# Kernel tuning notes

Measured on AMD Instinct MI355X. Metric: run time of the kernel, lower is better.

Reference implementation:

```python
import jax, jax.numpy as jnp
import numpy as np

HEADS = 4

def _pair_msg(H, w2, B, xsrc):
    # H:[E,mid] radial-MLP hidden; w2:[mid,co,ci,nf]; B:[E,m_out,m_in,nf] CG/SH basis; xsrc:[E,ci,m_in]
    tmp = jnp.einsum('epqf,eiq->eipf', B, xsrc)          # basis-weighted input  [E,ci,m_out,nf]
    R = jnp.einsum('eh,hoif->eoif', H, w2)               # per-edge radial weights [E,co,ci,nf]
    return jnp.einsum('eoif,eipf->eop', R, tmp)          # edge message [E,co,m_out]

def _conv_edges(ef, w1, w2_nf1, w2_11, b00, b01, b10, b11, x0s, x1s):
    # pair index p = 2*d_in + d_out; pairs (0,0),(0,1),(1,0) have nf=1, pair (1,1) has nf=3
    H = jax.nn.relu(jnp.einsum('ef,pfh->peh', ef, w1))
    m0 = _pair_msg(H[0], w2_nf1[0][..., None], b00, x0s) + _pair_msg(H[2], w2_nf1[2][..., None], b10, x1s)
    m1 = _pair_msg(H[1], w2_nf1[1][..., None], b01, x0s) + _pair_msg(H[3], w2_11, b11, x1s)
    return m0, m1

def _seg_softmax(z, dst, n):
    m = jax.ops.segment_max(z, dst, num_segments=n)
    m = jnp.where(jnp.isfinite(m), m, 0.0)
    e = jnp.exp(z - m[dst])
    s = jax.ops.segment_sum(e, dst, num_segments=n)
    return e / (s[dst] + 1e-9)

def _norm_se3(x, g, b, eps=1e-3):
    n = jnp.sqrt((x * x).sum(-1) + 1e-12)                # per-channel irrep norm [N,C]
    mu = n.mean(-1, keepdims=True)
    var = ((n - mu) ** 2).mean(-1, keepdims=True)
    ln = (n - mu) / jnp.sqrt(var + 1e-5) * g + b
    return x * (jax.nn.relu(ln) / (n + eps))[..., None]

def _forward(x0, x1, edge_feat, b00, b01, b10, b11, kv_w1, kv_w2_nf1, kv_w2_11,
             wq, wproj, norm_gamma, norm_beta, fc_w1, fc_w2_nf1, fc_w2_11, fc_wself,
             edge_src, edge_dst):
    N = x0.shape[0]
    E = edge_src.shape[0]
    L = kv_w1.shape[0]
    ckv = wq.shape[-1]
    scale = 1.0 / np.sqrt((ckv // HEADS) * 4)            # key feats per head over degrees 0,1 (1+3 comps)
    hs = lambda t: t.reshape(t.shape[0], HEADS, ckv // HEADS, t.shape[-1])
    for l in range(L):
        # AttentionBlockSE3: ConvSE3 -> per-edge key/value; LinearSE3 -> query; seg-softmax attention
        kv0, kv1 = _conv_edges(edge_feat, kv_w1[l], kv_w2_nf1[l], kv_w2_11[l],
                               b00, b01, b10, b11, x0[edge_src], x1[edge_src])
        k0, v0 = kv0[:, :ckv], kv0[:, ckv:]
        k1, v1 = kv1[:, :ckv], kv1[:, ckv:]
        q0 = jnp.einsum('ncm,cd->ndm', x0, wq[l, 0])
        q1 = jnp.einsum('ncm,cd->ndm', x1, wq[l, 1])
        z = (hs(q0)[edge_dst] * hs(k0)).sum((2, 3)) + (hs(q1)[edge_dst] * hs(k1)).sum((2, 3))
        alpha = _seg_softmax(z * scale, edge_dst, N)     # [E,heads]
        a0 = (alpha[:, :, None, None] * hs(v0)).reshape(E, ckv, 1)
        a1 = (alpha[:, :, None, None] * hs(v1)).reshape(E, ckv, 3)
        o0 = jax.ops.segment_sum(a0, edge_dst, num_segments=N)
        o1 = jax.ops.segment_sum(a1, edge_dst, num_segments=N)
        # project concat(attn_out, skip) per degree, then NormSE3
        x0 = jnp.einsum('ncm,cd->ndm', jnp.concatenate([o0, x0], 1), wproj[l, 0])
        x1 = jnp.einsum('ncm,cd->ndm', jnp.concatenate([o1, x1], 1), wproj[l, 1])
        x0 = _norm_se3(x0, norm_gamma[l, 0], norm_beta[l, 0])
        x1 = _norm_se3(x1, norm_gamma[l, 1], norm_beta[l, 1])
    # final ConvSE3 with self-interaction, scatter-aggregated over dst nodes
    m0, m1 = _conv_edges(edge_feat, fc_w1, fc_w2_nf1, fc_w2_11,
                         b00, b01, b10, b11, x0[edge_src], x1[edge_src])
    y0 = jax.ops.segment_sum(m0, edge_dst, num_segments=N) + jnp.einsum('ncm,cd->ndm', x0, fc_wself[0])
    y1 = jax.ops.segment_sum(m1, edge_dst, num_segments=N) + jnp.einsum('ncm,cd->ndm', x1, fc_wself[1])
    return jnp.concatenate([y0.reshape(N, -1), y1.reshape(N, -1)], axis=1)

def setup_inputs() -> dict:
    key = jax.random.key(0)
    ks = jax.random.split(key, 20)
    N, E, C, L = 8192, 131072, 16, 2
    Fe, mid, KV, ckv, Co = 16, 16, 16, 8, 8
    f = lambda k, s, sc=1.0: jax.random.normal(k, s, dtype=jnp.float32) * sc
    return {
        'x0': f(ks[0], (N, C, 1)),
        'x1': f(ks[1], (N, C, 3)),
        'edge_feat': f(ks[2], (E, Fe)),
        'b00': f(ks[3], (E, 1, 1, 1)),
        'b01': f(ks[4], (E, 3, 1, 1)),
        'b10': f(ks[5], (E, 1, 3, 1)),
        'b11': f(ks[6], (E, 3, 3, 3)),
        'kv_w1': f(ks[7], (L, 4, Fe, mid), 0.1),
        'kv_w2_nf1': f(ks[8], (L, 3, mid, KV, C), 0.1),
        'kv_w2_11': f(ks[9], (L, mid, KV, C, 3), 0.1),
        'wq': f(ks[10], (L, 2, C, ckv), 0.1),
        'wproj': f(ks[11], (L, 2, ckv + C, C), 0.1),
        'norm_gamma': jnp.ones((L, 2, C), dtype=jnp.float32),
        'norm_beta': jnp.zeros((L, 2, C), dtype=jnp.float32),
        'fc_w1': f(ks[12], (4, Fe, mid), 0.1),
        'fc_w2_nf1': f(ks[13], (3, mid, Co, C), 0.1),
        'fc_w2_11': f(ks[14], (mid, Co, C, 3), 0.1),
        'fc_wself': f(ks[15], (2, C, Co), 0.1),
        'edge_src': jax.random.randint(ks[16], (E,), 0, N, dtype=jnp.int32),
        'edge_dst': jax.random.randint(ks[17], (E,), 0, N, dtype=jnp.int32),
    }

def reference(x0, x1, edge_feat, b00, b01, b10, b11, kv_w1, kv_w2_nf1, kv_w2_11,
              wq, wproj, norm_gamma, norm_beta, fc_w1, fc_w2_nf1, fc_w2_11, fc_wself,
              edge_src, edge_dst):
    return _forward(x0, x1, edge_feat, b00, b01, b10, b11, kv_w1, kv_w2_nf1, kv_w2_11,
                    wq, wproj, norm_gamma, norm_beta, fc_w1, fc_w2_nf1, fc_w2_11, fc_wself,
                    edge_src, edge_dst)
```

## Files before the change

kernel.cpp:

```cpp
#include <hip/hip_runtime.h>
#include <hip/hip_fp16.h>
#include <math.h>


typedef _Float16 half8 __attribute__((ext_vector_type(8)));
typedef float f32x4 __attribute__((ext_vector_type(4)));

union AF {
    half8 h8;
    __half2 h2[4];
};
union U32h2 {
    unsigned u;
    __half2 h;
};

__global__ void k_hist(const int* __restrict__ dst, int* __restrict__ counts, int E) {
    int e = blockIdx.x * 256 + threadIdx.x;
    if (e < E) atomicAdd(&counts[dst[e]], 1);
}

__global__ __launch_bounds__(1024) void k_scan(const int* __restrict__ counts,
                                               int* __restrict__ rowptr,
                                               int* __restrict__ cursor,
                                               int N, int CH) {
    __shared__ int part[1024];
    int t = threadIdx.x;
    int s = 0;
    for (int i = 0; i < CH; ++i) {
        int idx = t * CH + i;
        if (idx < N) s += counts[idx];
    }
    part[t] = s;
    __syncthreads();
    for (int off = 1; off < 1024; off <<= 1) {
        int v = (t >= off) ? part[t - off] : 0;
        __syncthreads();
        part[t] += v;
        __syncthreads();
    }
    int run = (t == 0) ? 0 : part[t - 1];
    for (int i = 0; i < CH; ++i) {
        int idx = t * CH + i;
        if (idx < N) {
            rowptr[idx] = run;
            cursor[idx] = run;
            run += counts[idx];
        }
    }
    if (t == 0) rowptr[N] = part[1023];
}

__global__ void k_scatter(const int* __restrict__ dst, int* __restrict__ cursor,
                          int* __restrict__ pose, int E) {
    int e = blockIdx.x * 256 + threadIdx.x;
    if (e < E) {
        int pos = atomicAdd(&cursor[dst[e]], 1);
        pose[e] = pos;
    }
}

__global__ void k_misc(const float* __restrict__ x0, const float* __restrict__ x1,
                       const float* __restrict__ ef,
                       float* __restrict__ xs0, float* __restrict__ xs1,
                       unsigned short* __restrict__ efh, int n0, int n1, int n2) {
    int i = blockIdx.x * 256 + threadIdx.x;
    if (i < n0) xs0[i] = x0[i];
    else if (i < n0 + n1) xs1[i - n0] = x1[i - n0];
    else if (i < n0 + n1 + n2) {
        int k = i - n0 - n1;
        efh[k] = __half_as_ushort(__float2half(ef[k]));
    }
}

__global__ void k_prepw(const float* __restrict__ kvw1, const float* __restrict__ fcw1,
                        const float* __restrict__ kvw2n, const float* __restrict__ kvw211,
                        const float* __restrict__ fcw2n, const float* __restrict__ fcw211,
                        unsigned short* __restrict__ Wfrag) {
    int t = blockIdx.x * 256 + threadIdx.x;
    if (t >= 156 * 64 * 8) return;
    int j = t & 7;
    int lane = (t >> 3) & 63;
    int row = t >> 9;
    int quad = lane >> 4, m = lane & 15;
    int c = row / 52, r = row % 52;
    int KVO = (c < 2) ? 16 : 8;
    const float* w1src = (c < 2) ? (kvw1 + c * 1024) : fcw1;
    const float* w2n = (c < 2) ? (kvw2n + c * 12288) : fcw2n;
    const float* w211 = (c < 2) ? (kvw211 + c * 12288) : fcw211;
    float v = 0.f;
    if (r < 4) {
        if (quad < 2) v = w1src[r * 256 + (quad * 8 + j) * 16 + m];
    } else if (r < 28) {
        int fam = (r - 4) >> 3, kk = (r - 4) & 7;
        int h = quad * 4 + (j & 3), i = 2 * kk + (j >> 2);
        if (m < KVO) v = w2n[((fam * 16 + h) * KVO + m) * 16 + i];
    } else {
        int kk = r - 28;
        int h = quad * 4 + (j & 3);
        int ifx = 2 * kk + (j >> 2);
        int i = ifx / 3, f = ifx % 3;
        if (m < KVO) v = w211[((h * KVO + m) * 16 + i) * 3 + f];
    }
    Wfrag[t] = __half_as_ushort(__float2half(v));
}

template <int KVO, bool DO_Z>
__global__ __launch_bounds__(256) void k_conv(
    int E,
    const int* __restrict__ src, const int* __restrict__ dst,
    const int* __restrict__ pose,
    const float* __restrict__ xs0, const float* __restrict__ xs1,
    const float* __restrict__ b00, const float* __restrict__ b01,
    const float* __restrict__ b10, const float* __restrict__ b11,
    const unsigned short* __restrict__ efh,
    const unsigned short* __restrict__ Wfrag,
    int wbase,
    const float* __restrict__ q0, const float* __restrict__ q1,
    float* __restrict__ vrow, float* __restrict__ zb)
{
    __shared__ unsigned xBL[4][16 * 148];
    int tid = threadIdx.x;
    int wave = tid >> 6, lane = tid & 63;
    int tile = blockIdx.x * 4 + wave;
    if (tile * 16 >= E) return;
    int m = lane & 15, quad = lane >> 4;
    int e0 = tile * 16;
    int me = e0 + m;
    int s = src[me];
    unsigned* xw = xBL[wave];
    const half8* W8 = (const half8*)Wfrag;

    {
        float x1c[12];
        const float4* xp = (const float4*)(xs1 + (size_t)s * 48 + quad * 12);
#pragma unroll
        for (int cc = 0; cc < 3; ++cc) {
            float4 v = xp[cc];
            x1c[cc * 4 + 0] = v.x; x1c[cc * 4 + 1] = v.y;
            x1c[cc * 4 + 2] = v.z; x1c[cc * 4 + 3] = v.w;
        }
        float b11r[27];
#pragma unroll
        for (int k = 0; k < 27; ++k) b11r[k] = b11[(size_t)me * 27 + k];
#pragma unroll
        for (int p = 0; p < 3; ++p) {
            float vals[12];
#pragma unroll
            for (int i2 = 0; i2 < 4; ++i2) {
#pragma unroll
                for (int f = 0; f < 3; ++f) {
                    float a = 0.f;
#pragma unroll
                    for (int q = 0; q < 3; ++q) a += x1c[i2 * 3 + q] * b11r[p * 9 + q * 3 + f];
                    vals[i2 * 3 + f] = a;
                }
            }
#pragma unroll
            for (int cc = 0; cc < 3; ++cc) {
                unsigned uu[4];
#pragma unroll
                for (int i3 = 0; i3 < 4; ++i3) {
                    U32h2 u;
                    u.h = __float2half2_rn(vals[cc * 4 + i3]);
                    uu[i3] = u.u;
                }
                *(uint4*)&xw[m * 148 + p * 48 + quad * 12 + cc * 4] =
                    make_uint4(uu[0], uu[1], uu[2], uu[3]);
            }
        }
    }
    __syncthreads();

    __half2 x0d[16], t10d[16];
    {
        const float4* p = (const float4*)(xs0 + (size_t)s * 16);
#pragma unroll
        for (int k = 0; k < 4; ++k) {
            float4 v = p[k];
            x0d[k * 4 + 0] = __float2half2_rn(v.x);
            x0d[k * 4 + 1] = __float2half2_rn(v.y);
            x0d[k * 4 + 2] = __float2half2_rn(v.z);
            x0d[k * 4 + 3] = __float2half2_rn(v.w);
        }
        float bq0 = b10[(size_t)me * 3 + 0], bq1 = b10[(size_t)me * 3 + 1],
              bq2 = b10[(size_t)me * 3 + 2];
        const float4* xp = (const float4*)(xs1 + (size_t)s * 48);
#pragma unroll
        for (int g = 0; g < 4; ++g) {
            float4 a = xp[g * 3 + 0], b = xp[g * 3 + 1], cc = xp[g * 3 + 2];
            float xf[12] = {a.x, a.y, a.z, a.w, b.x, b.y, b.z, b.w, cc.x, cc.y, cc.z, cc.w};
#pragma unroll
            for (int i2 = 0; i2 < 4; ++i2)
                t10d[g * 4 + i2] = __float2half2_rn(
                    bq0 * xf[i2 * 3] + bq1 * xf[i2 * 3 + 1] + bq2 * xf[i2 * 3 + 2]);
        }
    }

    __half2 Hp2[4][2];
    {
        half8 efr = {0, 0, 0, 0, 0, 0, 0, 0};
        if (quad < 2) efr = *(const half8*)(efh + (size_t)me * 16 + quad * 8);
        f32x4 z4 = {0.f, 0.f, 0.f, 0.f};
#pragma unroll
        for (int pp = 0; pp < 4; ++pp) {
            half8 w1f = W8[(size_t)(wbase + pp) * 64 + lane];
            f32x4 hacc = __builtin_amdgcn_mfma_f32_16x16x32_f16(w1f, efr, z4, 0, 0, 0);
            Hp2[pp][0] = __float22half2_rn(
                make_float2(fmaxf(hacc[0], 0.f), fmaxf(hacc[1], 0.f)));
            Hp2[pp][1] = __float22half2_rn(
                make_float2(fmaxf(hacc[2], 0.f), fmaxf(hacc[3], 0.f)));
        }
    }

    f32x4 acc0 = {0.f, 0.f, 0.f, 0.f}, acc1 = acc0, acc2 = acc0;
    f32x4 accP0 = acc0, accP1 = acc0, accP2 = acc0;

#pragma unroll
    for (int kk = 0; kk < 8; ++kk) {
        __half2 xA = x0d[2 * kk], xB = x0d[2 * kk + 1];
        __half2 tA = t10d[2 * kk], tB = t10d[2 * kk + 1];
        AF a0, a1, a2;
        a0.h2[0] = __hmul2(Hp2[0][0], xA); a0.h2[1] = __hmul2(Hp2[0][1], xA);
        a0.h2[2] = __hmul2(Hp2[0][0], xB); a0.h2[3] = __hmul2(Hp2[0][1], xB);
        a1.h2[0] = __hmul2(Hp2[1][0], xA); a1.h2[1] = __hmul2(Hp2[1][1], xA);
        a1.h2[2] = __hmul2(Hp2[1][0], xB); a1.h2[3] = __hmul2(Hp2[1][1], xB);
        a2.h2[0] = __hmul2(Hp2[2][0], tA); a2.h2[1] = __hmul2(Hp2[2][1], tA);
        a2.h2[2] = __hmul2(Hp2[2][0], tB); a2.h2[3] = __hmul2(Hp2[2][1], tB);
        half8 w0 = W8[(size_t)(wbase + 4 + kk) * 64 + lane];
        half8 w1f = W8[(size_t)(wbase + 12 + kk) * 64 + lane];
        half8 w2f = W8[(size_t)(wbase + 20 + kk) * 64 + lane];
        acc0 = __builtin_amdgcn_mfma_f32_16x16x32_f16(w0, a0.h8, acc0, 0, 0, 0);
        acc1 = __builtin_amdgcn_mfma_f32_16x16x32_f16(w1f, a1.h8, acc1, 0, 0, 0);
        acc2 = __builtin_amdgcn_mfma_f32_16x16x32_f16(w2f, a2.h8, acc2, 0, 0, 0);
    }

#pragma unroll
    for (int kko = 0; kko < 12; ++kko) {
        uint4 xu0 = *(const uint4*)&xw[m * 148 + 0 * 48 + 4 * kko];
        uint4 xu1 = *(const uint4*)&xw[m * 148 + 1 * 48 + 4 * kko];
        uint4 xu2 = *(const uint4*)&xw[m * 148 + 2 * 48 + 4 * kko];
        unsigned qa0[4] = {xu0.x, xu0.y, xu0.z, xu0.w};
        unsigned qa1[4] = {xu1.x, xu1.y, xu1.z, xu1.w};
        unsigned qa2[4] = {xu2.x, xu2.y, xu2.z, xu2.w};
#pragma unroll
        for (int t = 0; t < 2; ++t) {
            U32h2 u;
            __half2 p0a, p0b, p1a, p1b, p2a, p2b;
            u.u = qa0[2 * t]; p0a = u.h; u.u = qa0[2 * t + 1]; p0b = u.h;
            u.u = qa1[2 * t]; p1a = u.h; u.u = qa1[2 * t + 1]; p1b = u.h;
            u.u = qa2[2 * t]; p2a = u.h; u.u = qa2[2 * t + 1]; p2b = u.h;
            AF a0, a1, a2;
            a0.h2[0] = __hmul2(Hp2[3][0], p0a); a0.h2[1] = __hmul2(Hp2[3][1], p0a);
            a0.h2[2] = __hmul2(Hp2[3][0], p0b); a0.h2[3] = __hmul2(Hp2[3][1], p0b);
            a1.h2[0] = __hmul2(Hp2[3][0], p1a); a1.h2[1] = __hmul2(Hp2[3][1], p1a);
            a1.h2[2] = __hmul2(Hp2[3][0], p1b); a1.h2[3] = __hmul2(Hp2[3][1], p1b);
            a2.h2[0] = __hmul2(Hp2[3][0], p2a); a2.h2[1] = __hmul2(Hp2[3][1], p2a);
            a2.h2[2] = __hmul2(Hp2[3][0], p2b); a2.h2[3] = __hmul2(Hp2[3][1], p2b);
            half8 wf = W8[(size_t)(wbase + 28 + 2 * kko + t) * 64 + lane];
            accP0 = __builtin_amdgcn_mfma_f32_16x16x32_f16(wf, a0.h8, accP0, 0, 0, 0);
            accP1 = __builtin_amdgcn_mfma_f32_16x16x32_f16(wf, a1.h8, accP1, 0, 0, 0);
            accP2 = __builtin_amdgcn_mfma_f32_16x16x32_f16(wf, a2.h8, accP2, 0, 0, 0);
        }
    }

    float b00r = b00[me];
    float b01r0 = b01[(size_t)me * 3 + 0], b01r1 = b01[(size_t)me * 3 + 1],
          b01r2 = b01[(size_t)me * 3 + 2];
    float o0v[4], o1v[4][3];
#pragma unroll
    for (int r = 0; r < 4; ++r) {
        o0v[r] = b00r * acc0[r] + acc2[r];
        o1v[r][0] = b01r0 * acc1[r] + accP0[r];
        o1v[r][1] = b01r1 * acc1[r] + accP1[r];
        o1v[r][2] = b01r2 * acc1[r] + accP2[r];
    }
    int pos = pose[me];
    bool doStore = DO_Z ? (quad >= 2) : (quad < 2);
    if (doStore) {
        int qa = DO_Z ? (quad - 2) : quad;
        float* vp = vrow + (size_t)pos * 32;
        *(float4*)&vp[qa * 4] = make_float4(o0v[0], o0v[1], o0v[2], o0v[3]);
        float* p1 = vp + 8 + qa * 12;
        *(float4*)&p1[0] = make_float4(o1v[0][0], o1v[0][1], o1v[0][2], o1v[1][0]);
        *(float4*)&p1[4] = make_float4(o1v[1][1], o1v[1][2], o1v[2][0], o1v[2][1]);
        *(float4*)&p1[8] = make_float4(o1v[2][2], o1v[3][0], o1v[3][1], o1v[3][2]);
    }
    if (DO_Z && quad < 2) {
        int n = dst[me];
        float4 q0v = *(const float4*)&q0[(size_t)n * 8 + quad * 4];
        const float4* q1p = (const float4*)&q1[(size_t)n * 24 + quad * 12];
        float4 qa4 = q1p[0], qb4 = q1p[1], qc4 = q1p[2];
        float q1f[12] = {qa4.x, qa4.y, qa4.z, qa4.w, qb4.x, qb4.y, qb4.z, qb4.w,
                         qc4.x, qc4.y, qc4.z, qc4.w};
        float q0f[4] = {q0v.x, q0v.y, q0v.z, q0v.w};
        float zh0 = 0.f, zh1 = 0.f;
#pragma unroll
        for (int r = 0; r < 4; ++r) {
            float tt = q0f[r] * o0v[r] + q1f[r * 3 + 0] * o1v[r][0] +
                       q1f[r * 3 + 1] * o1v[r][1] + q1f[r * 3 + 2] * o1v[r][2];
            if (r < 2) zh0 += tt;
            else zh1 += tt;
        }
        const float scale = 0.35355339059327373f;
        *(float2*)&zb[(size_t)pos * 4 + quad * 2] = make_float2(zh0 * scale, zh1 * scale);
    }
}

__global__ void k_q(int N, const float* __restrict__ xs0, const float* __restrict__ xs1,
                    const float* __restrict__ wq,
                    float* __restrict__ q0, float* __restrict__ q1) {
    int t = blockIdx.x * 256 + threadIdx.x;
    if (t >= N * 32) return;
    int n = t >> 5, comp = t & 31;
    if (comp < 8) {
        float a = 0.f;
#pragma unroll
        for (int c = 0; c < 16; ++c) a += xs0[n * 16 + c] * wq[c * 8 + comp];
        q0[n * 8 + comp] = a;
    } else {
        int idx = comp - 8, dd = idx / 3, mm = idx % 3;
        float a = 0.f;
#pragma unroll
        for (int c = 0; c < 16; ++c) a += xs1[n * 48 + c * 3 + mm] * wq[128 + c * 8 + dd];
        q1[n * 24 + dd * 3 + mm] = a;
    }
}

__global__ __launch_bounds__(256) void k_attn(
    int N,
    const int* __restrict__ rowptr,
    const float* __restrict__ zb, const float* __restrict__ vrow,
    const float* __restrict__ wproj,
    const float* __restrict__ gamma, const float* __restrict__ beta,
    float* __restrict__ xs0, float* __restrict__ xs1) {
    __shared__ float wpL[768];
    __shared__ float gL[32], btL[32];
    __shared__ float inb[16][100];
    __shared__ float aw[16][16][4];
    int tid = threadIdx.x;
    for (int i = tid; i < 768; i += 256) wpL[i] = wproj[i];
    if (tid < 32) { gL[tid] = gamma[tid]; btL[tid] = beta[tid]; }
    int wave = tid >> 6, lane = tid & 63;
    int sub = lane >> 4, l16 = lane & 15;
    int nodeIdx = wave * 4 + sub;
    int n = blockIdx.x * 16 + nodeIdx;
    if (n >= N) n = N - 1;
    int base = rowptr[n], deg = rowptr[n + 1] - base;
    const float4* zb4 = (const float4*)zb;

    float mx0 = -INFINITY, mx1 = -INFINITY, mx2 = -INFINITY, mx3 = -INFINITY;
    for (int j = l16; j < deg; j += 16) {
        float4 zv = zb4[base + j];
        mx0 = fmaxf(mx0, zv.x); mx1 = fmaxf(mx1, zv.y);
        mx2 = fmaxf(mx2, zv.z); mx3 = fmaxf(mx3, zv.w);
    }
#pragma unroll
    for (int off = 1; off < 16; off <<= 1) {
        mx0 = fmaxf(mx0, __shfl_xor(mx0, off));
        mx1 = fmaxf(mx1, __shfl_xor(mx1, off));
        mx2 = fmaxf(mx2, __shfl_xor(mx2, off));
        mx3 = fmaxf(mx3, __shfl_xor(mx3, off));
    }
    if (!isfinite(mx0)) mx0 = 0.f;
    if (!isfinite(mx1)) mx1 = 0.f;
    if (!isfinite(mx2)) mx2 = 0.f;
    if (!isfinite(mx3)) mx3 = 0.f;

    float s0 = 0.f, s1 = 0.f, s2 = 0.f, s3 = 0.f;
    for (int j = l16; j < deg; j += 16) {
        float4 zv = zb4[base + j];
        s0 += __expf(zv.x - mx0); s1 += __expf(zv.y - mx1);
        s2 += __expf(zv.z - mx2); s3 += __expf(zv.w - mx3);
    }
#pragma unroll
    for (int off = 1; off < 16; off <<= 1) {
        s0 += __shfl_xor(s0, off); s1 += __shfl_xor(s1, off);
        s2 += __shfl_xor(s2, off); s3 += __shfl_xor(s3, off);
    }
    float i0 = 1.f / (s0 + 1e-9f), i1 = 1.f / (s1 + 1e-9f);
    float i2 = 1.f / (s2 + 1e-9f), i3 = 1.f / (s3 + 1e-9f);

    int c0 = 2 * l16, c1 = c0 + 1;
    int hA = ((c0 < 8) ? c0 : (c0 - 8) / 3) >> 1;
    int hB = ((c1 < 8) ? c1 : (c1 - 8) / 3) >> 1;
    float accA = 0.f, accB = 0.f;
    for (int j0 = 0; j0 < deg; j0 += 16) {
        int j = j0 + l16;
        float4 a4 = make_float4(0.f, 0.f, 0.f, 0.f);
        if (j < deg) {
            float4 zv = zb4[base + j];
            a4.x = __expf(zv.x - mx0) * i0;
            a4.y = __expf(zv.y - mx1) * i1;
            a4.z = __expf(zv.z - mx2) * i2;
            a4.w = __expf(zv.w - mx3) * i3;
        }
        *(float4*)&aw[nodeIdx][l16][0] = a4;
        __builtin_amdgcn_wave_barrier();
        int cnt = min(16, deg - j0);
        for (int jj = 0; jj < cnt; ++jj) {
            float2 v = *(const float2*)&vrow[(size_t)(base + j0 + jj) * 32 + c0];
            accA += aw[nodeIdx][jj][hA] * v.x;
            accB += aw[nodeIdx][jj][hB] * v.y;
        }
        __builtin_amdgcn_wave_barrier();
    }

    float* in0 = inb[nodeIdx];
    float* in1 = in0 + 24;
    if (c0 < 8) { in0[c0] = accA; in0[c1] = accB; }
    else        { in1[c0 - 8] = accA; in1[c1 - 8] = accB; }
    in0[8 + l16] = xs0[(size_t)n * 16 + l16];
    {
        const float* xp = xs1 + (size_t)n * 48 + l16 * 3;
        in1[24 + l16 * 3 + 0] = xp[0];
        in1[24 + l16 * 3 + 1] = xp[1];
        in1[24 + l16 * 3 + 2] = xp[2];
    }
    __syncthreads();

    int c = l16;
    float y0 = 0.f;
#pragma unroll
    for (int j = 0; j < 24; ++j) y0 += in0[j] * wpL[j * 16 + c];
    float y1v[3];
#pragma unroll
    for (int mm = 0; mm < 3; ++mm) {
        float y = 0.f;
#pragma unroll
        for (int j = 0; j < 24; ++j) y += in1[j * 3 + mm] * wpL[384 + j * 16 + c];
        y1v[mm] = y;
    }
    float n0 = sqrtf(y0 * y0 + 1e-12f);
    float n1 = sqrtf(y1v[0] * y1v[0] + y1v[1] * y1v[1] + y1v[2] * y1v[2] + 1e-12f);
    float mu0 = n0, mu1 = n1;
#pragma unroll
    for (int off = 1; off < 16; off <<= 1) {
        mu0 += __shfl_xor(mu0, off);
        mu1 += __shfl_xor(mu1, off);
    }
    mu0 *= 0.0625f; mu1 *= 0.0625f;
    float dv0 = n0 - mu0, dv1 = n1 - mu1;
    float var0 = dv0 * dv0, var1 = dv1 * dv1;
#pragma unroll
    for (int off = 1; off < 16; off <<= 1) {
        var0 += __shfl_xor(var0, off);
        var1 += __shfl_xor(var1, off);
    }
    var0 *= 0.0625f; var1 *= 0.0625f;
    float ln0 = dv0 * rsqrtf(var0 + 1e-5f) * gL[c] + btL[c];
    float ln1 = dv1 * rsqrtf(var1 + 1e-5f) * gL[16 + c] + btL[16 + c];
    float fac0 = fmaxf(ln0, 0.f) / (n0 + 1e-3f);
    float fac1 = fmaxf(ln1, 0.f) / (n1 + 1e-3f);
    xs0[(size_t)n * 16 + c] = y0 * fac0;
    float* xo = xs1 + (size_t)n * 48 + c * 3;
    xo[0] = y1v[0] * fac1;
    xo[1] = y1v[1] * fac1;
    xo[2] = y1v[2] * fac1;
}

__global__ __launch_bounds__(256) void k_out(
    int N,
    const int* __restrict__ rowptr, const float* __restrict__ vrow,
    const float* __restrict__ xs0, const float* __restrict__ xs1,
    const float* __restrict__ wself,
    float* __restrict__ out) {
    int tid = threadIdx.x;
    int wave = tid >> 6, lane = tid & 63;
    int sub = lane >> 4, l16 = lane & 15;
    int n = blockIdx.x * 16 + wave * 4 + sub;
    if (n >= N) n = N - 1;
    int base = rowptr[n], deg = rowptr[n + 1] - base;

    int c0 = 2 * l16, c1 = c0 + 1;
    float accA = 0.f, accB = 0.f;
    for (int j = 0; j < deg; ++j) {
        float2 v = *(const float2*)&vrow[(size_t)(base + j) * 32 + c0];
        accA += v.x;
        accB += v.y;
    }
    if (c0 < 8) {
#pragma unroll
        for (int c = 0; c < 16; ++c) {
            float xv = xs0[(size_t)n * 16 + c];
            accA += xv * wself[c * 8 + c0];
            accB += xv * wself[c * 8 + c1];
        }
    } else {
        int dA = (c0 - 8) / 3, mA = (c0 - 8) % 3;
        int dB = (c1 - 8) / 3, mB = (c1 - 8) % 3;
#pragma unroll
        for (int c = 0; c < 16; ++c) {
            accA += xs1[(size_t)n * 48 + c * 3 + mA] * wself[128 + c * 8 + dA];
            accB += xs1[(size_t)n * 48 + c * 3 + mB] * wself[128 + c * 8 + dB];
        }
    }
    *(float2*)&out[(size_t)n * 32 + c0] = make_float2(accA, accB);
}

extern "C" void kernel_launch(void* const* d_in, const int* in_sizes, int n_in,
                              void* d_out, int out_size, void* d_ws, size_t ws_size,
                              hipStream_t stream) {
    const float* x0 = (const float*)d_in[0];
    const float* x1 = (const float*)d_in[1];
    const float* ef = (const float*)d_in[2];
    const float* b00 = (const float*)d_in[3];
    const float* b01 = (const float*)d_in[4];
    const float* b10 = (const float*)d_in[5];
    const float* b11 = (const float*)d_in[6];
    const float* kvw1 = (const float*)d_in[7];
    const float* kvw2n = (const float*)d_in[8];
    const float* kvw211 = (const float*)d_in[9];
    const float* wq = (const float*)d_in[10];
    const float* wproj = (const float*)d_in[11];
    const float* gam = (const float*)d_in[12];
    const float* bet = (const float*)d_in[13];
    const float* fcw1 = (const float*)d_in[14];
    const float* fcw2n = (const float*)d_in[15];
    const float* fcw211 = (const float*)d_in[16];
    const float* fcself = (const float*)d_in[17];
    const int* esrc = (const int*)d_in[18];
    const int* edst = (const int*)d_in[19];
    int N = in_sizes[0] / 16;
    int E = in_sizes[18];
    float* out = (float*)d_out;

    float* ws = (float*)d_ws;
    size_t off = 0;
    float* xs0 = ws + off; off += (size_t)N * 16;
    float* xs1 = ws + off; off += (size_t)N * 48;
    float* q0b = ws + off; off += (size_t)N * 8;
    float* q1b = ws + off; off += (size_t)N * 24;
    float* vrow = ws + off; off += (size_t)E * 32;
    float* zb = ws + off; off += (size_t)E * 4;
    int* counts = (int*)(ws + off); off += N;
    int* rowptr = (int*)(ws + off); off += N + 1;
    int* cursor = (int*)(ws + off); off += N;
    int* pose = (int*)(ws + off); off += E;
    off = (off + 3) & ~(size_t)3;
    unsigned short* efh = (unsigned short*)(ws + off); off += (size_t)E * 16 / 2;
    unsigned short* Wfrag = (unsigned short*)(ws + off); off += (size_t)156 * 64 * 8 / 2;

    const int tpb = 256;
    int ebl = (E + 255) / 256;
    int cblk = (E / 16 + 3) / 4;
    int nbl16 = (N + 15) / 16;

    k_prepw<<<(156 * 512 + 255) / 256, tpb, 0, stream>>>(kvw1, fcw1, kvw2n, kvw211,
                                                         fcw2n, fcw211, Wfrag);
    int mtot = N * 64 + E * 16;
    k_misc<<<(mtot + 255) / 256, tpb, 0, stream>>>(x0, x1, ef, xs0, xs1, efh,
                                                   N * 16, N * 48, E * 16);
    hipMemsetAsync(counts, 0, (size_t)N * 4, stream);
    k_hist<<<ebl, tpb, 0, stream>>>(edst, counts, E);
    int CH = (N + 1023) / 1024;
    k_scan<<<1, 1024, 0, stream>>>(counts, rowptr, cursor, N, CH);
    k_scatter<<<ebl, tpb, 0, stream>>>(edst, cursor, pose, E);

    for (int l = 0; l < 2; ++l) {
        k_q<<<(N * 32 + 255) / 256, tpb, 0, stream>>>(N, xs0, xs1, wq + l * 256, q0b, q1b);
        k_conv<16, true><<<cblk, tpb, 0, stream>>>(E, esrc, edst, pose, xs0, xs1,
                                                   b00, b01, b10, b11, efh, Wfrag, l * 52,
                                                   q0b, q1b, vrow, zb);
        k_attn<<<nbl16, tpb, 0, stream>>>(N, rowptr, zb, vrow, wproj + l * 768,
                                          gam + l * 32, bet + l * 32, xs0, xs1);
    }
    k_conv<8, false><<<cblk, tpb, 0, stream>>>(E, esrc, edst, pose, xs0, xs1,
                                               b00, b01, b10, b11, efh, Wfrag, 2 * 52,
                                               q0b, q1b, vrow, zb);
    k_out<<<nbl16, tpb, 0, stream>>>(N, rowptr, vrow, xs0, xs1, fcself, out);
}
```

Measured before the change: 295.2 us.

## Repack conv MFMA operands, fuse next-layer query into attention, unroll gathers

Changes the MFMA B-fragment layout so each half2 pair carries two input channels instead of a duplicated scalar, which halves the LDS staging buffer and the per-edge register arrays in the conv kernel. Fuses the second layer's query projection into the epilogue of the first attention kernel, removing one k_q launch and a reread of the node features. Unrolls the per-node value gather loops in the attention and output kernels by four to expose more memory-level parallelism. The weight-prep permutation has to match the new operand packing exactly, and the fused query path depends on the shared buffers in k_attn holding the right values.

Result: no change. 292.9 us (-0.8%).

```diff
diff --git a/kernel.cpp b/kernel.cpp
--- a/kernel.cpp
+++ b/kernel.cpp
@@ -93,12 +93,12 @@
         if (quad < 2) v = w1src[r * 256 + (quad * 8 + j) * 16 + m];
     } else if (r < 28) {
         int fam = (r - 4) >> 3, kk = (r - 4) & 7;
-        int h = quad * 4 + (j & 3), i = 2 * kk + (j >> 2);
+        int h = quad * 4 + ((j >> 1) & 3), i = 2 * kk + (j & 1);
         if (m < KVO) v = w2n[((fam * 16 + h) * KVO + m) * 16 + i];
     } else {
-        int kk = r - 28;
-        int h = quad * 4 + (j & 3);
-        int ifx = 2 * kk + (j >> 2);
+        int kk2 = r - 28;
+        int h = quad * 4 + ((j >> 1) & 3);
+        int ifx = 2 * kk2 + (j & 1);
         int i = ifx / 3, f = ifx % 3;
         if (m < KVO) v = w211[((h * KVO + m) * 16 + i) * 3 + f];
     }
@@ -119,7 +119,7 @@
     const float* __restrict__ q0, const float* __restrict__ q1,
     float* __restrict__ vrow, float* __restrict__ zb)
 {
-    __shared__ unsigned xBL[4][16 * 148];
+    __shared__ __align__(16) unsigned xBL[4][16 * 74];
     int tid = threadIdx.x;
     int wave = tid >> 6, lane = tid & 63;
     int tile = blockIdx.x * 4 + wave;
@@ -156,48 +156,48 @@
                     vals[i2 * 3 + f] = a;
                 }
             }
-#pragma unroll
-            for (int cc = 0; cc < 3; ++cc) {
-                unsigned uu[4];
-#pragma unroll
-                for (int i3 = 0; i3 < 4; ++i3) {
-                    U32h2 u;
-                    u.h = __float2half2_rn(vals[cc * 4 + i3]);
-                    uu[i3] = u.u;
-                }
-                *(uint4*)&xw[m * 148 + p * 48 + quad * 12 + cc * 4] =
-                    make_uint4(uu[0], uu[1], uu[2], uu[3]);
+            unsigned uu[6];
+#pragma unroll
+            for (int u = 0; u < 6; ++u) {
+                U32h2 w;
+                w.h = __float22half2_rn(make_float2(vals[2 * u], vals[2 * u + 1]));
+                uu[u] = w.u;
             }
+            int boff = m * 74 + p * 24 + quad * 6;
+            *(uint2*)&xw[boff + 0] = make_uint2(uu[0], uu[1]);
+            *(uint2*)&xw[boff + 2] = make_uint2(uu[2], uu[3]);
+            *(uint2*)&xw[boff + 4] = make_uint2(uu[4], uu[5]);
         }
     }
     __syncthreads();
 
-    __half2 x0d[16], t10d[16];
+    __half2 x0p[8], t10p[8];
     {
         const float4* p = (const float4*)(xs0 + (size_t)s * 16);
 #pragma unroll
         for (int k = 0; k < 4; ++k) {
             float4 v = p[k];
-            x0d[k * 4 + 0] = __float2half2_rn(v.x);
-            x0d[k * 4 + 1] = __float2half2_rn(v.y);
-            x0d[k * 4 + 2] = __float2half2_rn(v.z);
-            x0d[k * 4 + 3] = __float2half2_rn(v.w);
+            x0p[2 * k + 0] = __float22half2_rn(make_float2(v.x, v.y));
+            x0p[2 * k + 1] = __float22half2_rn(make_float2(v.z, v.w));
         }
         float bq0 = b10[(size_t)me * 3 + 0], bq1 = b10[(size_t)me * 3 + 1],
               bq2 = b10[(size_t)me * 3 + 2];
         const float4* xp = (const float4*)(xs1 + (size_t)s * 48);
+        float tf[16];
 #pragma unroll
         for (int g = 0; g < 4; ++g) {
             float4 a = xp[g * 3 + 0], b = xp[g * 3 + 1], cc = xp[g * 3 + 2];
             float xf[12] = {a.x, a.y, a.z, a.w, b.x, b.y, b.z, b.w, cc.x, cc.y, cc.z, cc.w};
 #pragma unroll
             for (int i2 = 0; i2 < 4; ++i2)
-                t10d[g * 4 + i2] = __float2half2_rn(
-                    bq0 * xf[i2 * 3] + bq1 * xf[i2 * 3 + 1] + bq2 * xf[i2 * 3 + 2]);
-        }
-    }
-
-    __half2 Hp2[4][2];
+                tf[g * 4 + i2] = bq0 * xf[i2 * 3] + bq1 * xf[i2 * 3 + 1] + bq2 * xf[i2 * 3 + 2];
+        }
+#pragma unroll
+        for (int k = 0; k < 8; ++k)
+            t10p[k] = __float22half2_rn(make_float2(tf[2 * k], tf[2 * k + 1]));
+    }
+
+    __half2 Hd[4][4];
     {
         half8 efr = {0, 0, 0, 0, 0, 0, 0, 0};
         if (quad < 2) efr = *(const half8*)(efh + (size_t)me * 16 + quad * 8);
@@ -206,10 +206,9 @@
         for (int pp = 0; pp < 4; ++pp) {
             half8 w1f = W8[(size_t)(wbase + pp) * 64 + lane];
             f32x4 hacc = __builtin_amdgcn_mfma_f32_16x16x32_f16(w1f, efr, z4, 0, 0, 0);
-            Hp2[pp][0] = __float22half2_rn(
-                make_float2(fmaxf(hacc[0], 0.f), fmaxf(hacc[1], 0.f)));
-            Hp2[pp][1] = __float22half2_rn(
-                make_float2(fmaxf(hacc[2], 0.f), fmaxf(hacc[3], 0.f)));
+#pragma unroll
+            for (int r = 0; r < 4; ++r)
+                Hd[pp][r] = __float2half2_rn(__float2half(fmaxf(hacc[r], 0.f)));
         }
     }
 
@@ -218,15 +217,14 @@
 
 #pragma unroll
     for (int kk = 0; kk < 8; ++kk) {
-        __half2 xA = x0d[2 * kk], xB = x0d[2 * kk + 1];
-        __half2 tA = t10d[2 * kk], tB = t10d[2 * kk + 1];
+        __half2 xp_ = x0p[kk], tp_ = t10p[kk];
         AF a0, a1, a2;
-        a0.h2[0] = __hmul2(Hp2[0][0], xA); a0.h2[1] = __hmul2(Hp2[0][1], xA);
-        a0.h2[2] = __hmul2(Hp2[0][0], xB); a0.h2[3] = __hmul2(Hp2[0][1], xB);
-        a1.h2[0] = __hmul2(Hp2[1][0], xA); a1.h2[1] = __hmul2(Hp2[1][1], xA);
-        a1.h2[2] = __hmul2(Hp2[1][0], xB); a1.h2[3] = __hmul2(Hp2[1][1], xB);
-        a2.h2[0] = __hmul2(Hp2[2][0], tA); a2.h2[1] = __hmul2(Hp2[2][1], tA);
-        a2.h2[2] = __hmul2(Hp2[2][0], tB); a2.h2[3] = __hmul2(Hp2[2][1], tB);
+#pragma unroll
+        for (int t = 0; t < 4; ++t) {
+            a0.h2[t] = __hmul2(Hd[0][t], xp_);
+            a1.h2[t] = __hmul2(Hd[1][t], xp_);
+            a2.h2[t] = __hmul2(Hd[2][t], tp_);
+        }
         half8 w0 = W8[(size_t)(wbase + 4 + kk) * 64 + lane];
         half8 w1f = W8[(size_t)(wbase + 12 + kk) * 64 + lane];
         half8 w2f = W8[(size_t)(wbase + 20 + kk) * 64 + lane];
@@ -237,26 +235,23 @@
 
 #pragma unroll
     for (int kko = 0; kko < 12; ++kko) {
-        uint4 xu0 = *(const uint4*)&xw[m * 148 + 0 * 48 + 4 * kko];
-        uint4 xu1 = *(const uint4*)&xw[m * 148 + 1 * 48 + 4 * kko];
-        uint4 xu2 = *(const uint4*)&xw[m * 148 + 2 * 48 + 4 * kko];
-        unsigned qa0[4] = {xu0.x, xu0.y, xu0.z, xu0.w};
-        unsigned qa1[4] = {xu1.x, xu1.y, xu1.z, xu1.w};
-        unsigned qa2[4] = {xu2.x, xu2.y, xu2.z, xu2.w};
+        uint2 xu0 = *(const uint2*)&xw[m * 74 + 0 * 24 + 2 * kko];
+        uint2 xu1 = *(const uint2*)&xw[m * 74 + 1 * 24 + 2 * kko];
+        uint2 xu2 = *(const uint2*)&xw[m * 74 + 2 * 24 + 2 * kko];
+        unsigned pv0[2] = {xu0.x, xu0.y};
+        unsigned pv1[2] = {xu1.x, xu1.y};
+        unsigned pv2[2] = {xu2.x, xu2.y};
 #pragma unroll
         for (int t = 0; t < 2; ++t) {
-            U32h2 u;
-            __half2 p0a, p0b, p1a, p1b, p2a, p2b;
-            u.u = qa0[2 * t]; p0a = u.h; u.u = qa0[2 * t + 1]; p0b = u.h;
-            u.u = qa1[2 * t]; p1a = u.h; u.u = qa1[2 * t + 1]; p1b = u.h;
-            u.u = qa2[2 * t]; p2a = u.h; u.u = qa2[2 * t + 1]; p2b = u.h;
+            U32h2 u0, u1, u2;
+            u0.u = pv0[t]; u1.u = pv1[t]; u2.u = pv2[t];
             AF a0, a1, a2;
-            a0.h2[0] = __hmul2(Hp2[3][0], p0a); a0.h2[1] = __hmul2(Hp2[3][1], p0a);
-            a0.h2[2] = __hmul2(Hp2[3][0], p0b); a0.h2[3] = __hmul2(Hp2[3][1], p0b);
-            a1.h2[0] = __hmul2(Hp2[3][0], p1a); a1.h2[1] = __hmul2(Hp2[3][1], p1a);
-            a1.h2[2] = __hmul2(Hp2[3][0], p1b); a1.h2[3] = __hmul2(Hp2[3][1], p1b);
-            a2.h2[0] = __hmul2(Hp2[3][0], p2a); a2.h2[1] = __hmul2(Hp2[3][1], p2a);
-            a2.h2[2] = __hmul2(Hp2[3][0], p2b); a2.h2[3] = __hmul2(Hp2[3][1], p2b);
+#pragma unroll
+            for (int r = 0; r < 4; ++r) {
+                a0.h2[r] = __hmul2(Hd[3][r], u0.h);
+                a1.h2[r] = __hmul2(Hd[3][r], u1.h);
+                a2.h2[r] = __hmul2(Hd[3][r], u2.h);
+            }
             half8 wf = W8[(size_t)(wbase + 28 + 2 * kko + t) * 64 + lane];
             accP0 = __builtin_amdgcn_mfma_f32_16x16x32_f16(wf, a0.h8, accP0, 0, 0, 0);
             accP1 = __builtin_amdgcn_mfma_f32_16x16x32_f16(wf, a1.h8, accP1, 0, 0, 0);
@@ -333,7 +328,9 @@
     const float* __restrict__ zb, const float* __restrict__ vrow,
     const float* __restrict__ wproj,
     const float* __restrict__ gamma, const float* __restrict__ beta,
-    float* __restrict__ xs0, float* __restrict__ xs1) {
+    float* __restrict__ xs0, float* __restrict__ xs1,
+    const float* __restrict__ wq_next,
+    float* __restrict__ q0, float* __restrict__ q1) {
     __shared__ float wpL[768];
     __shared__ float gL[32], btL[32];
     __shared__ float inb[16][100];
@@ -398,8 +395,20 @@
         *(float4*)&aw[nodeIdx][l16][0] = a4;
         __builtin_amdgcn_wave_barrier();
         int cnt = min(16, deg - j0);
-        for (int jj = 0; jj < cnt; ++jj) {
-            float2 v = *(const float2*)&vrow[(size_t)(base + j0 + jj) * 32 + c0];
+        const float* vbase = &vrow[(size_t)(base + j0) * 32 + c0];
+        int jj = 0;
+        for (; jj + 3 < cnt; jj += 4) {
+            float2 v0 = *(const float2*)(vbase + (size_t)jj * 32);
+            float2 v1 = *(const float2*)(vbase + (size_t)(jj + 1) * 32);
+            float2 v2 = *(const float2*)(vbase + (size_t)(jj + 2) * 32);
+            float2 v3 = *(const float2*)(vbase + (size_t)(jj + 3) * 32);
+            accA += aw[nodeIdx][jj][hA] * v0.x + aw[nodeIdx][jj + 1][hA] * v1.x +
+                    aw[nodeIdx][jj + 2][hA] * v2.x + aw[nodeIdx][jj + 3][hA] * v3.x;
+            accB += aw[nodeIdx][jj][hB] * v0.y + aw[nodeIdx][jj + 1][hB] * v1.y +
+                    aw[nodeIdx][jj + 2][hB] * v2.y + aw[nodeIdx][jj + 3][hB] * v3.y;
+        }
+        for (; jj < cnt; ++jj) {
+            float2 v = *(const float2*)(vbase + (size_t)jj * 32);
             accA += aw[nodeIdx][jj][hA] * v.x;
             accB += aw[nodeIdx][jj][hB] * v.y;
         }
@@ -452,11 +461,38 @@
     float ln1 = dv1 * rsqrtf(var1 + 1e-5f) * gL[16 + c] + btL[16 + c];
     float fac0 = fmaxf(ln0, 0.f) / (n0 + 1e-3f);
     float fac1 = fmaxf(ln1, 0.f) / (n1 + 1e-3f);
-    xs0[(size_t)n * 16 + c] = y0 * fac0;
+    float x0n = y0 * fac0;
+    float x1n[3] = {y1v[0] * fac1, y1v[1] * fac1, y1v[2] * fac1};
+    xs0[(size_t)n * 16 + c] = x0n;
     float* xo = xs1 + (size_t)n * 48 + c * 3;
-    xo[0] = y1v[0] * fac1;
-    xo[1] = y1v[1] * fac1;
-    xo[2] = y1v[2] * fac1;
+    xo[0] = x1n[0]; xo[1] = x1n[1]; xo[2] = x1n[2];
+
+    if (wq_next) {
+        __builtin_amdgcn_wave_barrier();
+        in0[8 + c] = x0n;
+        in1[24 + c * 3 + 0] = x1n[0];
+        in1[24 + c * 3 + 1] = x1n[1];
+        in1[24 + c * 3 + 2] = x1n[2];
+        __builtin_amdgcn_wave_barrier();
+        int compA = 2 * l16, compB = compA + 1;
+#pragma unroll
+        for (int cb = 0; cb < 2; ++cb) {
+            int comp = cb ? compB : compA;
+            float a = 0.f;
+            if (comp < 8) {
+#pragma unroll
+                for (int cc = 0; cc < 16; ++cc)
+                    a += in0[8 + cc] * wq_next[cc * 8 + comp];
+                q0[(size_t)n * 8 + comp] = a;
+            } else {
+                int idx = comp - 8, dd = idx / 3, mm = idx % 3;
+#pragma unroll
+                for (int cc = 0; cc < 16; ++cc)
+                    a += in1[24 + cc * 3 + mm] * wq_next[128 + cc * 8 + dd];
+                q1[(size_t)n * 24 + idx] = a;
+            }
+        }
+    }
 }
 
 __global__ __launch_bounds__(256) void k_out(
@@ -474,8 +510,18 @@
 
     int c0 = 2 * l16, c1 = c0 + 1;
     float accA = 0.f, accB = 0.f;
-    for (int j = 0; j < deg; ++j) {
-        float2 v = *(const float2*)&vrow[(size_t)(base + j) * 32 + c0];
+    const float* vbase = &vrow[(size_t)base * 32 + c0];
+    int j = 0;
+    for (; j + 3 < deg; j += 4) {
+        float2 v0 = *(const float2*)(vbase + (size_t)j * 32);
+        float2 v1 = *(const float2*)(vbase + (size_t)(j + 1) * 32);
+        float2 v2 = *(const float2*)(vbase + (size_t)(j + 2) * 32);
+        float2 v3 = *(const float2*)(vbase + (size_t)(j + 3) * 32);
+        accA += v0.x + v1.x + v2.x + v3.x;
+        accB += v0.y + v1.y + v2.y + v3.y;
+    }
+    for (; j < deg; ++j) {
+        float2 v = *(const float2*)(vbase + (size_t)j * 32);
         accA += v.x;
         accB += v.y;
     }
@@ -556,17 +602,20 @@
     int CH = (N + 1023) / 1024;
     k_scan<<<1, 1024, 0, stream>>>(counts, rowptr, cursor, N, CH);
     k_scatter<<<ebl, tpb, 0, stream>>>(edst, cursor, pose, E);
-
-    for (int l = 0; l < 2; ++l) {
-        k_q<<<(N * 32 + 255) / 256, tpb, 0, stream>>>(N, xs0, xs1, wq + l * 256, q0b, q1b);
-        k_conv<16, true><<<cblk, tpb, 0, stream>>>(E, esrc, edst, pose, xs0, xs1,
-                                                   b00, b01, b10, b11, efh, Wfrag, l * 52,
-                                                   q0b, q1b, vrow, zb);
-        k_attn<<<nbl16, tpb, 0, stream>>>(N, rowptr, zb, vrow, wproj + l * 768,
-                                          gam + l * 32, bet + l * 32, xs0, xs1);
-    }
+    k_q<<<(N * 32 + 255) / 256, tpb, 0, stream>>>(N, xs0, xs1, wq, q0b, q1b);
+
+    k_conv<16, true><<<cblk, tpb, 0, stream>>>(E, esrc, edst, pose, xs0, xs1,
+                                               b00, b01, b10, b11, efh, Wfrag, 0,
+                                               q0b, q1b, vrow, zb);
+    k_attn<<<nbl16, tpb, 0, stream>>>(N, rowptr, zb, vrow, wproj,
+                                      gam, bet, xs0, xs1, wq + 256, q0b, q1b);
+    k_conv<16, true><<<cblk, tpb, 0, stream>>>(E, esrc, edst, pose, xs0, xs1,
+                                               b00, b01, b10, b11, efh, Wfrag, 52,
+                                               q0b, q1b, vrow, zb);
+    k_attn<<<nbl16, tpb, 0, stream>>>(N, rowptr, zb, vrow, wproj + 768,
+                                      gam + 32, bet + 32, xs0, xs1, nullptr, q0b, q1b);
     k_conv<8, false><<<cblk, tpb, 0, stream>>>(E, esrc, edst, pose, xs0, xs1,
-                                               b00, b01, b10, b11, efh, Wfrag, 2 * 52,
+                                               b00, b01, b10, b11, efh, Wfrag, 104,
                                                q0b, q1b, vrow, zb);
     k_out<<<nbl16, tpb, 0, stream>>>(N, rowptr, vrow, xs0, xs1, fcself, out);
 }
```
